# Kernel optimization log

Measured on AMD Instinct MI355X. Metric: run time of the kernel, lower is better.

Reference implementation:

```python
import jax, jax.numpy as jnp
from jax import lax
import numpy as np

# Straight-through-estimator sign (standard BNN binarization):
# fwd: sign(x) with sign(0)=+1; bwd: pass gradient where |x|<=1 (hardtanh STE).
@jax.custom_vjp
def sign_ste(x):
    return jnp.where(x >= 0, 1.0, -1.0).astype(x.dtype)

def _sign_fwd(x):
    return sign_ste(x), x

def _sign_bwd(x, g):
    return (g * (jnp.abs(x) <= 1.0).astype(g.dtype),)

sign_ste.defvjp(_sign_fwd, _sign_bwd)

EPS = 1e-5  # BatchNorm eps (torch default)

def bn4(x, g, b):  # BatchNorm2d, training-mode batch stats, x: [N,C,H,W]
    m = x.mean((0, 2, 3), keepdims=True)
    v = x.var((0, 2, 3), keepdims=True)
    return g[None, :, None, None] * (x - m) * lax.rsqrt(v + EPS) + b[None, :, None, None]

def bn1(x, g, b):  # BatchNorm1d, x: [N,C]
    m = x.mean(0, keepdims=True)
    v = x.var(0, keepdims=True)
    return g * (x - m) * lax.rsqrt(v + EPS) + b

def bconv(x, W, b, first):
    # BinarizedConv2d: binarize weights always; binarize input except first layer.
    xb = x if first else sign_ste(x)
    y = lax.conv_general_dilated(xb, sign_ste(W), (1, 1), [(1, 1), (1, 1)],
                                 dimension_numbers=('NCHW', 'OIHW', 'NCHW'))
    return y + b[None, :, None, None]

def maxpool2(x):
    return lax.reduce_window(x, -jnp.inf, lax.max, (1, 1, 2, 2), (1, 1, 2, 2), 'VALID')

def ht(x):  # Hardtanh
    return jnp.clip(x, -1.0, 1.0)

CONV_CH = [(3, 64), (64, 128), (128, 256), (256, 256), (256, 512), (512, 512), (512, 512), (512, 512)]
LIN_CH = [(512, 512), (512, 512), (512, 10)]
POOL_AFTER = (0, 1, 3, 5, 7)  # conv indices followed by MaxPool2d

def setup_inputs():
    key = jax.random.key(0)
    ks = iter(jax.random.split(key, 64))
    d = {"x": jax.random.normal(next(ks), (256, 3, 32, 32), jnp.float32)}
    for i, (ci, co) in enumerate(CONV_CH):
        d[f"cw{i}"] = jax.random.normal(next(ks), (co, ci, 3, 3), jnp.float32) * 0.1
        d[f"cb{i}"] = jnp.zeros((co,), jnp.float32)
        d[f"cg{i}"] = jnp.ones((co,), jnp.float32)
        d[f"ct{i}"] = jnp.zeros((co,), jnp.float32)
    for i, (ci, co) in enumerate(LIN_CH):
        d[f"lw{i}"] = jax.random.normal(next(ks), (co, ci), jnp.float32) * 0.1
        d[f"lb{i}"] = jnp.zeros((co,), jnp.float32)
        d[f"lg{i}"] = jnp.ones((co,), jnp.float32)
        d[f"lt{i}"] = jnp.zeros((co,), jnp.float32)
    return d

def _forward(x, cw, cb, cg, ct, lw, lb, lg, lt):
    h = x
    for i in range(8):
        h = bconv(h, cw[i], cb[i], i == 0)
        if i in POOL_AFTER:
            h = maxpool2(h)
        h = ht(bn4(h, cg[i], ct[i]))
    h = h.reshape(h.shape[0], -1)  # [N, 512] after 5 pools on 32x32
    for i in range(3):
        h = sign_ste(h) @ sign_ste(lw[i]).T + lb[i]  # BinarizedLinear
        h = bn1(h, lg[i], lt[i])
        if i < 2:
            h = ht(h)  # Dropout is identity in eval mode
    return jax.nn.log_softmax(h, axis=-1)

def reference(x,
              cw0, cb0, cg0, ct0, cw1, cb1, cg1, ct1, cw2, cb2, cg2, ct2,
              cw3, cb3, cg3, ct3, cw4, cb4, cg4, ct4, cw5, cb5, cg5, ct5,
              cw6, cb6, cg6, ct6, cw7, cb7, cg7, ct7,
              lw0, lb0, lg0, lt0, lw1, lb1, lg1, lt1, lw2, lb2, lg2, lt2):
    cw = [cw0, cw1, cw2, cw3, cw4, cw5, cw6, cw7]
    cb = [cb0, cb1, cb2, cb3, cb4, cb5, cb6, cb7]
    cg = [cg0, cg1, cg2, cg3, cg4, cg5, cg6, cg7]
    ct = [ct0, ct1, ct2, ct3, ct4, ct5, ct6, ct7]
    lw = [lw0, lw1, lw2]
    lb = [lb0, lb1, lb2]
    lg = [lg0, lg1, lg2]
    lt = [lt0, lt1, lt2]
    return _forward(x, cw, cb, cg, ct, lw, lb, lg, lt)
```

## Files before the change

### kernel.cpp

```cpp
#include <hip/hip_runtime.h>
#include <hip/hip_bf16.h>

typedef unsigned long long u64;

#define EPSV 1e-5

__device__ __forceinline__ int imax(int a, int b) { return a > b ? a : b; }
__device__ __forceinline__ int iclamp(int v, int lo, int hi) { return v < lo ? lo : (v > hi ? hi : v); }

struct PrepArgs {
    const float* src[10];
    u64* dst[10];
    int CW[10];
    int Co[10];
    int taps[10];
    int rowbase[11];
    u64* accs;
    int naccs;
};

__global__ __launch_bounds__(256) void prep_kernel(PrepArgs a) {
    __shared__ float buf[4608];
    const int blk = blockIdx.x;
    int z = blk * 18 + threadIdx.x;
    if (threadIdx.x < 18 && z < a.naccs) a.accs[z] = 0ULL;

    int l = 0;
    while (l < 9 && blk >= a.rowbase[l + 1]) ++l;
    const int row = blk - a.rowbase[l];
    const int CW = a.CW[l];
    const int taps = a.taps[l];
    const int nf = CW * 64 * taps;
    const float* srow = a.src[l] + (size_t)row * nf;
    for (int i = threadIdx.x; i < nf; i += 256) buf[i] = srow[i];
    __syncthreads();
    const int t = threadIdx.x;
    if (t < taps * CW) {
        u64 bits = 0;
        if (taps == 9) {
            int k = t % 9, w = t / 9;
            for (int j = 0; j < 64; ++j) bits |= (u64)(buf[(w * 64 + j) * 9 + k] >= 0.f) << j;
            a.dst[l][(size_t)(k * CW + w) * a.Co[l] + row] = bits;
        } else {
            for (int j = 0; j < 64; ++j) bits |= (u64)(buf[t * 64 + j] >= 0.f) << j;
            a.dst[l][(size_t)row * CW + t] = bits;
        }
    }
}

__global__ __launch_bounds__(256) void conv0_lane(const float* __restrict__ x,
                                                  const float* __restrict__ wgt,
                                                  float* __restrict__ out,
                                                  double* __restrict__ dacc) {
    const int lane = threadIdx.x & 63;
    const int wave = threadIdx.x >> 6;
    float ws[27];
#pragma unroll
    for (int j = 0; j < 27; ++j) ws[j] = (wgt[lane * 27 + j] >= 0.f) ? 1.f : -1.f;

    const int gp0 = blockIdx.x * 32;
    const int n = gp0 >> 8;
    const int ypA = (gp0 >> 4) & 15;
    const int yb = 2 * ypA - 1;

    __shared__ float simg[3][6][34];
    const float* xb = x + (size_t)n * 3072;
    for (int t = threadIdx.x; t < 612; t += 256) {
        int ci = t / 204;
        int rem = t % 204;
        int r = rem / 34;
        int cc = rem % 34;
        int yy = yb + r;
        int xx = cc - 1;
        float v = 0.f;
        if ((unsigned)yy < 32u && (unsigned)xx < 32u) v = xb[(ci * 32 + yy) * 32 + xx];
        simg[ci][r][cc] = v;
    }
    __syncthreads();

    double s1 = 0.0, s2 = 0.0;
#pragma unroll 2
    for (int pi = 0; pi < 8; ++pi) {
        const int lp = wave * 8 + pi;
        const int gp = gp0 + lp;
        const int xp = lp & 15;
        const int rbase = 2 * (lp >> 4);
        const int cbase = 2 * xp;
        float win[3][4][4];
#pragma unroll
        for (int ci = 0; ci < 3; ++ci)
#pragma unroll
            for (int r = 0; r < 4; ++r)
#pragma unroll
                for (int c = 0; c < 4; ++c) win[ci][r][c] = simg[ci][rbase + r][cbase + c];
        float a00 = 0.f, a01 = 0.f, a10 = 0.f, a11 = 0.f;
#pragma unroll
        for (int ci = 0; ci < 3; ++ci)
#pragma unroll
            for (int ky = 0; ky < 3; ++ky)
#pragma unroll
                for (int kx = 0; kx < 3; ++kx) {
                    float wv = ws[ci * 9 + ky * 3 + kx];
                    a00 += win[ci][ky][kx] * wv;
                    a01 += win[ci][ky][kx + 1] * wv;
                    a10 += win[ci][ky + 1][kx] * wv;
                    a11 += win[ci][ky + 1][kx + 1] * wv;
                }
        float val = fmaxf(fmaxf(a00, a01), fmaxf(a10, a11));
        out[(size_t)gp * 64 + lane] = val;
        s1 += (double)val;
        s2 += (double)val * (double)val;
    }
    __shared__ double sh1[4][64], sh2[4][64];
    sh1[wave][lane] = s1;
    sh2[wave][lane] = s2;
    __syncthreads();
    if (threadIdx.x < 64) {
        double t1 = 0.0, t2 = 0.0;
#pragma unroll
        for (int r = 0; r < 4; ++r) { t1 += sh1[r][threadIdx.x]; t2 += sh2[r][threadIdx.x]; }
        double* sh = dacc + (size_t)(blockIdx.x & 7) * 1024;
        atomicAdd(&sh[2 * threadIdx.x], t1);
        atomicAdd(&sh[2 * threadIdx.x + 1], t2);
    }
}

__global__ __launch_bounds__(256) void bnpack_f(const float* __restrict__ in,
                                                const double* __restrict__ dacc,
                                                const float* __restrict__ g,
                                                const float* __restrict__ b,
                                                u64* __restrict__ act, int count) {
    __shared__ float2 sthr[64];
    if (threadIdx.x < 64) {
        int i = threadIdx.x;
        double S1 = 0.0, S2 = 0.0;
#pragma unroll
        for (int s = 0; s < 8; ++s) {
            S1 += dacc[s * 1024 + 2 * i];
            S2 += dacc[s * 1024 + 2 * i + 1];
        }
        double m = S1 / count;
        double var = S2 / count - m * m;
        double sc = (double)g[i] / sqrt(var + EPSV);
        float2 r;
        if (sc == 0.0) r = make_float2(b[i] >= 0.f ? -3.0e38f : 3.0e38f, 1.f);
        else {
            double t = m - (double)b[i] / sc;
            r = make_float2((float)t, sc > 0.0 ? 1.f : -1.f);
        }
        sthr[i] = r;
    }
    __syncthreads();
    int tid = blockIdx.x * 256 + threadIdx.x;
    int part = tid & 3;
    int word = tid >> 2;
    const float4* r4 = (const float4*)(in + (size_t)word * 64 + part * 16);
    u64 bits = 0;
#pragma unroll
    for (int q = 0; q < 4; ++q) {
        float4 v = r4[q];
        float vv[4] = {v.x, v.y, v.z, v.w};
#pragma unroll
        for (int u = 0; u < 4; ++u) {
            int c = part * 16 + q * 4 + u;
            float2 t = sthr[c];
            bool bit = (t.y > 0.f) ? (vv[u] >= t.x) : (vv[u] <= t.x);
            bits |= (u64)bit << c;
        }
    }
    bits |= __shfl_xor(bits, 1);
    bits |= __shfl_xor(bits, 2);
    if (part == 0) act[word] = bits;
}

__global__ __launch_bounds__(256) void bnpack_i(const short* __restrict__ in,
                                                const u64* __restrict__ iacc,
                                                const float* __restrict__ g,
                                                const float* __restrict__ b,
                                                u64* __restrict__ act, int Co, int wshift,
                                                int count) {
    __shared__ int2 sthr[520];
    for (int i = threadIdx.x; i < Co; i += 256) {
        long long S1 = 0, S2 = 0;
#pragma unroll
        for (int s = 0; s < 8; ++s) {
            S1 += (long long)iacc[s * 1024 + 2 * i];
            S2 += (long long)iacc[s * 1024 + 2 * i + 1];
        }
        double m = (double)S1 / count;
        double var = (double)S2 / count - m * m;
        double sc = (double)g[i] / sqrt(var + EPSV);
        int2 r;
        if (sc == 0.0) r = make_int2(b[i] >= 0.f ? (int)0x80000000 : 0x7fffffff, 0);
        else {
            double t = m - (double)b[i] / sc;
            if (t > 1.0e9) t = 1.0e9;
            if (t < -1.0e9) t = -1.0e9;
            r = (sc > 0.0) ? make_int2((int)ceil(t), 0) : make_int2((int)floor(t), 1);
        }
        sthr[(i >> 6) * 65 + (i & 63)] = r;
    }
    __syncthreads();
    int tid = blockIdx.x * 256 + threadIdx.x;
    int part = tid & 3;
    int word = tid >> 2;
    int w = word & ((1 << wshift) - 1);
    int pix = word >> wshift;
    const int4* r4 = (const int4*)(in + (size_t)pix * Co + (w << 6) + part * 16);
    u64 bits = 0;
#pragma unroll
    for (int q = 0; q < 2; ++q) {
        int4 v = r4[q];
        int words4[4] = {v.x, v.y, v.z, v.w};
#pragma unroll
        for (int u = 0; u < 4; ++u) {
#pragma unroll
            for (int h = 0; h < 2; ++h) {
                int c = part * 16 + q * 8 + u * 2 + h;
                int val = (int)(short)((h == 0) ? (words4[u] & 0xffff) : ((unsigned)words4[u] >> 16));
                int2 t = sthr[w * 65 + c];
                bool bit = t.y ? (val <= t.x) : (val >= t.x);
                bits |= (u64)bit << c;
            }
        }
    }
    bits |= __shfl_xor(bits, 1);
    bits |= __shfl_xor(bits, 2);
    if (part == 0) act[word] = bits;
}

template <int CW, int HIN, bool POOL, int WC, bool INTERIOR>
__device__ __forceinline__ void row_accum(const u64* __restrict__ inb,
                                          const u64* __restrict__ wpkT, int Co, int co,
                                          const int* yoff, const bool* ry, int* acc) {
    constexpr int HP = POOL ? HIN / 2 : HIN;
    constexpr int WS = POOL ? 4 : 3;
    constexpr int NA = POOL ? 4 : 1;
#pragma unroll 1
    for (int w0 = 0; w0 < CW; w0 += WC) {
        u64 wg[9 * WC];
#pragma unroll
        for (int k = 0; k < 9; ++k)
#pragma unroll
            for (int w = 0; w < WC; ++w)
                wg[k * WC + w] = wpkT[(size_t)(k * CW + w0 + w) * Co + co];
        u64 cur[WS][WS][WC];
#pragma unroll
        for (int d = 0; d < WS; ++d) {
            int cc = d - 1;
            int ccc = cc < 0 ? 0 : cc;
#pragma unroll
            for (int r = 0; r < WS; ++r) {
                const u64* p = inb + yoff[r] + ccc * CW + w0;
                if (WC == 1) {
                    cur[r][d][0] = p[0];
                } else {
                    ulonglong2 v = *(const ulonglong2*)p;
                    cur[r][d][0] = v.x;
                    cur[r][d][1] = v.y;
                }
            }
        }
#pragma unroll
        for (int xp = 0; xp < HP; ++xp) {
            if constexpr (POOL) {
#pragma unroll
                for (int py = 0; py < 2; ++py)
#pragma unroll
                    for (int qx = 0; qx < 2; ++qx)
#pragma unroll
                        for (int ky = 0; ky < 3; ++ky)
#pragma unroll
                            for (int kx = 0; kx < 3; ++kx) {
                                int d = qx + kx;
                                int cc = 2 * xp + d - 1;
                                if (cc >= 0 && cc < HIN) {
#pragma unroll
                                    for (int w = 0; w < WC; ++w) {
                                        int pcv = 64 - 2 * (int)__popcll(cur[py + ky][d][w] ^
                                                                         wg[(ky * 3 + kx) * WC + w]);
                                        if constexpr (INTERIOR)
                                            acc[xp * NA + py * 2 + qx] += pcv;
                                        else
                                            acc[xp * NA + py * 2 + qx] += ry[py + ky] ? pcv : 0;
                                    }
                                }
                            }
            } else {
#pragma unroll
                for (int ky = 0; ky < 3; ++ky)
#pragma unroll
                    for (int kx = 0; kx < 3; ++kx) {
                        int cc = xp + kx - 1;
                        if (cc >= 0 && cc < HIN) {
#pragma unroll
                            for (int w = 0; w < WC; ++w) {
                                int pcv = 64 - 2 * (int)__popcll(cur[ky][kx][w] ^
                                                                 wg[(ky * 3 + kx) * WC + w]);
                                if constexpr (INTERIOR)
                                    acc[xp] += pcv;
                                else
                                    acc[xp] += ry[ky] ? pcv : 0;
                            }
                        }
                    }
            }
            if (xp < HP - 1) {
                if constexpr (POOL) {
#pragma unroll
                    for (int r = 0; r < WS; ++r)
#pragma unroll
                        for (int w = 0; w < WC; ++w) {
                            cur[r][0][w] = cur[r][2][w];
                            cur[r][1][w] = cur[r][3][w];
                        }
#pragma unroll
                    for (int dd = 2; dd < 4; ++dd) {
                        int cc = 2 * (xp + 1) + dd - 1;
                        int ccc = cc >= HIN ? HIN - 1 : cc;
#pragma unroll
                        for (int r = 0; r < WS; ++r) {
                            const u64* p = inb + yoff[r] + ccc * CW + w0;
                            if (WC == 1) {
                                cur[r][dd][0] = p[0];
                            } else {
                                ulonglong2 v = *(const ulonglong2*)p;
                                cur[r][dd][0] = v.x;
                                cur[r][dd][1] = v.y;
                            }
                        }
                    }
                } else {
#pragma unroll
                    for (int r = 0; r < WS; ++r)
#pragma unroll
                        for (int w = 0; w < WC; ++w) {
                            cur[r][0][w] = cur[r][1][w];
                            cur[r][1][w] = cur[r][2][w];
                        }
                    int cc = xp + 2;
                    int ccc = cc >= HIN ? HIN - 1 : cc;
#pragma unroll
                    for (int r = 0; r < WS; ++r) {
                        const u64* p = inb + yoff[r] + ccc * CW + w0;
                        if (WC == 1) {
                            cur[r][2][0] = p[0];
                        } else {
                            ulonglong2 v = *(const ulonglong2*)p;
                            cur[r][2][0] = v.x;
                            cur[r][2][1] = v.y;
                        }
                    }
                }
            }
        }
    }
}

template <int CW, int HIN, bool POOL, int WC>
__global__ __launch_bounds__(256) void bconv_row(const u64* __restrict__ in,
                                                 const u64* __restrict__ wpkT,
                                                 short* __restrict__ out,
                                                 u64* __restrict__ iacc, int Co) {
    constexpr int HP = POOL ? HIN / 2 : HIN;
    constexpr int WS = POOL ? 4 : 3;
    constexpr int NA = POOL ? 4 : 1;
    const int lane = threadIdx.x & 63;
    const int co = blockIdx.y * 64 + lane;
    const int grow = blockIdx.x * 4 + (threadIdx.x >> 6);
    const int n = grow / HP;
    const int yp = grow % HP;
    const int y0 = (POOL ? 2 * yp : yp) - 1;
    const u64* inb = in + (size_t)n * (HIN * HIN * CW);
    int yoff[WS];
    bool ry[WS];
#pragma unroll
    for (int r = 0; r < WS; ++r) {
        int y = y0 + r;
        ry[r] = (unsigned)y < (unsigned)HIN;
        int yc = iclamp(y, 0, HIN - 1);
        yoff[r] = yc * HIN * CW;
    }
    int acc[HP * NA];
#pragma unroll
    for (int i = 0; i < HP * NA; ++i) acc[i] = 0;

    if (yp > 0 && yp < HP - 1)
        row_accum<CW, HIN, POOL, WC, true>(inb, wpkT, Co, co, yoff, ry, acc);
    else
        row_accum<CW, HIN, POOL, WC, false>(inb, wpkT, Co, co, yoff, ry, acc);

    int s1 = 0;
    long long s2 = 0;
    short* orow = out + (size_t)grow * HP * Co + co;
#pragma unroll
    for (int xp = 0; xp < HP; ++xp) {
        int ival;
        if constexpr (POOL)
            ival = imax(imax(acc[xp * 4], acc[xp * 4 + 1]), imax(acc[xp * 4 + 2], acc[xp * 4 + 3]));
        else
            ival = acc[xp];
        orow[(size_t)xp * Co] = (short)ival;
        s1 += ival;
        s2 += (long long)ival * ival;
    }

    __shared__ u64 sacc[128];
    if (threadIdx.x < 128) sacc[threadIdx.x] = 0ULL;
    __syncthreads();
    atomicAdd(&sacc[lane], (u64)(long long)s1);
    atomicAdd(&sacc[64 + lane], (u64)s2);
    __syncthreads();
    u64* sh = iacc + (size_t)(blockIdx.x & 7) * 1024;
    if (threadIdx.x < 64)
        atomicAdd(&sh[2 * (blockIdx.y * 64 + threadIdx.x)], sacc[threadIdx.x]);
    else if (threadIdx.x < 128)
        atomicAdd(&sh[2 * (blockIdx.y * 64 + threadIdx.x - 64) + 1], sacc[threadIdx.x]);
}

template <int CW, int HIN, bool POOL>
__global__ __launch_bounds__(256) void bconv_tiny(const u64* __restrict__ in,
                                                  const u64* __restrict__ wpkT,
                                                  short* __restrict__ out,
                                                  u64* __restrict__ iacc, int Co) {
    constexpr int NPX = HIN * HIN;
    constexpr int HP = POOL ? HIN / 2 : HIN;
    const int lane = threadIdx.x & 63;
    const int co = blockIdx.y * 64 + lane;
    const int n = blockIdx.x * 4 + (threadIdx.x >> 6);
    const u64* inb = in + (size_t)n * CW * NPX;
    int acc[NPX];
#pragma unroll
    for (int i = 0; i < NPX; ++i) acc[i] = 0;

#pragma unroll 2
    for (int w = 0; w < CW; ++w) {
        u64 win[NPX];
#pragma unroll
        for (int i = 0; i < NPX; ++i) win[i] = inb[i * CW + w];
#pragma unroll
        for (int k = 0; k < 9; ++k) {
            u64 wb = wpkT[(size_t)(k * CW + w) * Co + co];
            const int ky = k / 3, kx = k % 3;
#pragma unroll
            for (int py = 0; py < HIN; ++py)
#pragma unroll
                for (int px = 0; px < HIN; ++px) {
                    const int yy = py + ky - 1, xx = px + kx - 1;
                    if (yy >= 0 && yy < HIN && xx >= 0 && xx < HIN)
                        acc[py * HIN + px] += 64 - 2 * (int)__popcll(win[yy * HIN + xx] ^ wb);
                }
        }
    }

    short vals[HP * HP];
    if constexpr (POOL) {
#pragma unroll
        for (int py = 0; py < HP; ++py)
#pragma unroll
            for (int px = 0; px < HP; ++px)
                vals[py * HP + px] = (short)imax(
                    imax(acc[(2 * py) * HIN + 2 * px], acc[(2 * py) * HIN + 2 * px + 1]),
                    imax(acc[(2 * py + 1) * HIN + 2 * px], acc[(2 * py + 1) * HIN + 2 * px + 1]));
    } else {
#pragma unroll
        for (int i = 0; i < NPX; ++i) vals[i] = (short)acc[i];
    }
#pragma unroll
    for (int p = 0; p < HP * HP; ++p) out[(size_t)(n * HP * HP + p) * Co + co] = vals[p];

    long long s1 = 0, s2 = 0;
#pragma unroll
    for (int p = 0; p < HP * HP; ++p) {
        s1 += vals[p];
        s2 += (long long)vals[p] * vals[p];
    }
    __shared__ u64 sacc[128];
    if (threadIdx.x < 128) sacc[threadIdx.x] = 0ULL;
    __syncthreads();
    atomicAdd(&sacc[lane], (u64)s1);
    atomicAdd(&sacc[64 + lane], (u64)s2);
    __syncthreads();
    u64* sh = iacc + (size_t)(blockIdx.x & 7) * 1024;
    if (threadIdx.x < 64)
        atomicAdd(&sh[2 * (blockIdx.y * 64 + threadIdx.x)], sacc[threadIdx.x]);
    else if (threadIdx.x < 128)
        atomicAdd(&sh[2 * (blockIdx.y * 64 + threadIdx.x - 64) + 1], sacc[threadIdx.x]);
}

__global__ __launch_bounds__(256) void lin_kernel(const u64* __restrict__ hp,
                                                  const u64* __restrict__ wp,
                                                  const float* __restrict__ lb,
                                                  const float* __restrict__ g,
                                                  const float* __restrict__ bta,
                                                  float* __restrict__ z, int O, int applyHt) {
    int o = blockIdx.x;
    int n = threadIdx.x;
    const u64* hr = hp + n * 8;
    const u64* wr = wp + o * 8;
    int s = 0;
#pragma unroll
    for (int w = 0; w < 8; ++w) s += (int)__popcll(hr[w] ^ wr[w]);
    float val = (float)(512 - 2 * s) + lb[o];
    __shared__ double sh1[256], sh2[256];
    sh1[n] = (double)val;
    sh2[n] = (double)val * (double)val;
    __syncthreads();
    for (int st = 128; st > 0; st >>= 1) {
        if (n < st) {
            sh1[n] += sh1[n + st];
            sh2[n] += sh2[n + st];
        }
        __syncthreads();
    }
    __shared__ float sm, siv;
    if (n == 0) {
        double m = sh1[0] / 256.0;
        double var = sh2[0] / 256.0 - m * m;
        sm = (float)m;
        siv = (float)(1.0 / sqrt(var + EPSV));
    }
    __syncthreads();
    float zz = g[o] * (val - sm) * siv + bta[o];
    if (applyHt) zz = fminf(1.f, fmaxf(-1.f, zz));
    z[(size_t)n * O + o] = zz;
}

__global__ void pack_rows(const float* __restrict__ z, u64* __restrict__ hp) {
    int tid = blockIdx.x * 256 + threadIdx.x;
    int part = tid & 3;
    int word = tid >> 2;
    int ww = word & 7;
    int n = word >> 3;
    const float4* r4 = (const float4*)(z + (size_t)n * 512 + (ww << 6) + part * 16);
    u64 bits = 0;
#pragma unroll
    for (int q = 0; q < 4; ++q) {
        float4 v = r4[q];
        float vv[4] = {v.x, v.y, v.z, v.w};
#pragma unroll
        for (int u = 0; u < 4; ++u) bits |= (u64)(vv[u] >= 0.f) << (part * 16 + q * 4 + u);
    }
    bits |= __shfl_xor(bits, 1);
    bits |= __shfl_xor(bits, 2);
    if (part == 0) hp[word] = bits;
}

__global__ void lsm_kernel(const float* __restrict__ z, float* __restrict__ out) {
    int n = blockIdx.x * 64 + threadIdx.x;
    if (n >= 256) return;
    float v[10];
    float m = -1e30f;
#pragma unroll
    for (int i = 0; i < 10; ++i) {
        v[i] = z[n * 10 + i];
        m = fmaxf(m, v[i]);
    }
    float s = 0.f;
#pragma unroll
    for (int i = 0; i < 10; ++i) s += expf(v[i] - m);
    float ls = logf(s);
#pragma unroll
    for (int i = 0; i < 10; ++i) out[n * 10 + i] = v[i] - m - ls;
}

extern "C" void kernel_launch(void* const* d_in, const int* in_sizes, int n_in, void* d_out,
                              int out_size, void* d_ws, size_t ws_size, hipStream_t stream) {
    (void)in_sizes; (void)n_in; (void)out_size; (void)ws_size;
    const float* x = (const float*)d_in[0];
    const float *cw[8], *cb[8], *cg[8], *ct[8];
    for (int i = 0; i < 8; ++i) {
        cw[i] = (const float*)d_in[1 + 4 * i];
        cb[i] = (const float*)d_in[2 + 4 * i];
        cg[i] = (const float*)d_in[3 + 4 * i];
        ct[i] = (const float*)d_in[4 + 4 * i];
    }
    const float *lw[3], *lb[3], *lg[3], *lt[3];
    for (int i = 0; i < 3; ++i) {
        lw[i] = (const float*)d_in[33 + 4 * i];
        lb[i] = (const float*)d_in[34 + 4 * i];
        lg[i] = (const float*)d_in[35 + 4 * i];
        lt[i] = (const float*)d_in[36 + 4 * i];
    }

    static const int CIs[8] = {3, 64, 128, 256, 256, 512, 512, 512};
    static const int COs[8] = {64, 128, 256, 256, 512, 512, 512, 512};
    static const int HPs[8] = {16, 8, 8, 4, 4, 2, 2, 1};

    char* ws = (char*)d_ws;
    size_t off = 0;
    auto alloc = [&](size_t bytes) -> void* {
        void* p = ws + off;
        off += (bytes + 255) & ~(size_t)255;
        return p;
    };

    u64* wpkT[8] = {};
    for (int i = 1; i < 8; ++i) wpkT[i] = (u64*)alloc((size_t)COs[i] * 9 * (CIs[i] / 64) * 8);
    u64* wpl[3];
    int LO[3] = {512, 512, 10};
    for (int i = 0; i < 3; ++i) wpl[i] = (u64*)alloc((size_t)LO[i] * 8 * 8);
    u64* act[8];
    for (int i = 0; i < 8; ++i) act[i] = (u64*)alloc((size_t)256 * (COs[i] / 64) * HPs[i] * HPs[i] * 8);
    u64* fcs0 = (u64*)alloc(2048 * 8);
    u64* fcs1 = (u64*)alloc(2048 * 8);
    float* out0 = (float*)alloc((size_t)65536 * 64 * 4);
    short* i16A = (short*)alloc((size_t)16384 * 256 * 2);
    short* i16B = (short*)alloc((size_t)16384 * 256 * 2);
    float* z0 = (float*)alloc((size_t)256 * 512 * 4);
    float* z1 = (float*)alloc((size_t)256 * 512 * 4);
    float* z2 = (float*)alloc((size_t)256 * 10 * 4);
    u64* accs = (u64*)alloc((size_t)8 * 8 * 1024 * 8);
    double* dacc0 = (double*)accs;
    auto iacc = [&](int layer) { return accs + (size_t)layer * 8192; };

    PrepArgs pa;
    int rb = 0;
    for (int i = 1; i < 8; ++i) {
        int e = i - 1;
        pa.src[e] = cw[i];
        pa.dst[e] = wpkT[i];
        pa.CW[e] = CIs[i] / 64;
        pa.Co[e] = COs[i];
        pa.taps[e] = 9;
        pa.rowbase[e] = rb;
        rb += COs[i];
    }
    for (int i = 0; i < 3; ++i) {
        int e = 7 + i;
        pa.src[e] = lw[i];
        pa.dst[e] = wpl[i];
        pa.CW[e] = 8;
        pa.Co[e] = LO[i];
        pa.taps[e] = 1;
        pa.rowbase[e] = rb;
        rb += LO[i];
    }
    pa.rowbase[10] = rb;
    pa.accs = accs;
    pa.naccs = 8 * 8 * 1024;
    prep_kernel<<<rb, 256, 0, stream>>>(pa);

    conv0_lane<<<2048, 256, 0, stream>>>(x, cw[0], out0, dacc0);
    bnpack_f<<<1024, 256, 0, stream>>>(out0, dacc0, cg[0], ct[0], act[0], 65536);

    bconv_row<1, 16, true, 1><<<dim3(512, 2), 256, 0, stream>>>(act[0], wpkT[1], i16A, iacc(1), 128);
    bnpack_i<<<512, 256, 0, stream>>>(i16A, iacc(1), cg[1], ct[1], act[1], 128, 1, 16384);

    bconv_row<2, 8, false, 2><<<dim3(512, 4), 256, 0, stream>>>(act[1], wpkT[2], i16B, iacc(2), 256);
    bnpack_i<<<1024, 256, 0, stream>>>(i16B, iacc(2), cg[2], ct[2], act[2], 256, 2, 16384);

    bconv_row<4, 8, true, 2><<<dim3(256, 4), 256, 0, stream>>>(act[2], wpkT[3], i16A, iacc(3), 256);
    bnpack_i<<<256, 256, 0, stream>>>(i16A, iacc(3), cg[3], ct[3], act[3], 256, 2, 4096);

    bconv_row<4, 4, false, 2><<<dim3(256, 8), 256, 0, stream>>>(act[3], wpkT[4], i16B, iacc(4), 512);
    bnpack_i<<<512, 256, 0, stream>>>(i16B, iacc(4), cg[4], ct[4], act[4], 512, 3, 4096);

    bconv_tiny<8, 4, true><<<dim3(64, 8), 256, 0, stream>>>(act[4], wpkT[5], i16A, iacc(5), 512);
    bnpack_i<<<128, 256, 0, stream>>>(i16A, iacc(5), cg[5], ct[5], act[5], 512, 3, 1024);

    bconv_tiny<8, 2, false><<<dim3(64, 8), 256, 0, stream>>>(act[5], wpkT[6], i16B, iacc(6), 512);
    bnpack_i<<<128, 256, 0, stream>>>(i16B, iacc(6), cg[6], ct[6], act[6], 512, 3, 1024);

    bconv_tiny<8, 2, true><<<dim3(64, 8), 256, 0, stream>>>(act[6], wpkT[7], i16A, iacc(7), 512);
    bnpack_i<<<32, 256, 0, stream>>>(i16A, iacc(7), cg[7], ct[7], act[7], 512, 3, 256);

    lin_kernel<<<512, 256, 0, stream>>>(act[7], wpl[0], lb[0], lg[0], lt[0], z0, 512, 1);
    pack_rows<<<32, 256, 0, stream>>>(z0, fcs0);
    lin_kernel<<<512, 256, 0, stream>>>(fcs0, wpl[1], lb[1], lg[1], lt[1], z1, 512, 1);
    pack_rows<<<32, 256, 0, stream>>>(z1, fcs1);
    lin_kernel<<<10, 256, 0, stream>>>(fcs1, wpl[2], lb[2], lg[2], lt[2], z2, 10, 0);
    lsm_kernel<<<4, 64, 0, stream>>>(z2, (float*)d_out);
}
```

Before: 393.8 us.

## Restructure conv0 sliding window, count-only popcount accumulation, fuse linear tail kernels

conv0 now stages weights in shared memory and lets each wave slide a register window along a row, reusing overlapping columns instead of reloading the full window per pixel. The binary conv kernels accumulate raw popcounts and apply the 64*CW*taps - 2*cnt correction once per output, which drops the per-tap arithmetic. The linear layers write sign bits straight into packed words with atomicOr, so the pack_rows kernels go away, and the last linear layer is merged with BN and log_softmax into a single block. The accumulator-zeroing in prep is widened to also clear the packed FC buffers.

After: 425.8 us. +8.1%, slower.

```diff
diff --git a/kernel.cpp b/kernel.cpp
--- a/kernel.cpp
+++ b/kernel.cpp
@@ -22,8 +22,8 @@
 __global__ __launch_bounds__(256) void prep_kernel(PrepArgs a) {
     __shared__ float buf[4608];
     const int blk = blockIdx.x;
-    int z = blk * 18 + threadIdx.x;
-    if (threadIdx.x < 18 && z < a.naccs) a.accs[z] = 0ULL;
+    int z = blk * 19 + threadIdx.x;
+    if (threadIdx.x < 19 && z < a.naccs) a.accs[z] = 0ULL;
 
     int l = 0;
     while (l < 9 && blk >= a.rowbase[l + 1]) ++l;
@@ -54,16 +54,17 @@
                                                   double* __restrict__ dacc) {
     const int lane = threadIdx.x & 63;
     const int wave = threadIdx.x >> 6;
-    float ws[27];
-#pragma unroll
-    for (int j = 0; j < 27; ++j) ws[j] = (wgt[lane * 27 + j] >= 0.f) ? 1.f : -1.f;
+
+    __shared__ __align__(16) float simg[3 * 6 * 34];
+    __shared__ float swgt[64 * 27];
 
     const int gp0 = blockIdx.x * 32;
     const int n = gp0 >> 8;
     const int ypA = (gp0 >> 4) & 15;
     const int yb = 2 * ypA - 1;
 
-    __shared__ float simg[3][6][34];
+    for (int t = threadIdx.x; t < 1728; t += 256) swgt[t] = wgt[t];
+
     const float* xb = x + (size_t)n * 3072;
     for (int t = threadIdx.x; t < 612; t += 256) {
         int ci = t / 204;
@@ -74,25 +75,35 @@
         int xx = cc - 1;
         float v = 0.f;
         if ((unsigned)yy < 32u && (unsigned)xx < 32u) v = xb[(ci * 32 + yy) * 32 + xx];
-        simg[ci][r][cc] = v;
-    }
-    __syncthreads();
+        simg[(ci * 6 + r) * 34 + cc] = v;
+    }
+    __syncthreads();
+
+    float ws[27];
+#pragma unroll
+    for (int j = 0; j < 27; ++j) ws[j] = (swgt[lane * 27 + j] >= 0.f) ? 1.f : -1.f;
+
+    const int wr = wave >> 1;
+    const int xh = (wave & 1) * 8;
+    const int rb = 2 * wr;
+
+    float win[3][4][4];
+#pragma unroll
+    for (int ci = 0; ci < 3; ++ci)
+#pragma unroll
+        for (int r = 0; r < 4; ++r) {
+            const float2* p = (const float2*)&simg[(ci * 6 + rb + r) * 34 + 2 * xh];
+            float2 a = p[0], b = p[1];
+            win[ci][r][0] = a.x;
+            win[ci][r][1] = a.y;
+            win[ci][r][2] = b.x;
+            win[ci][r][3] = b.y;
+        }
 
     double s1 = 0.0, s2 = 0.0;
-#pragma unroll 2
-    for (int pi = 0; pi < 8; ++pi) {
-        const int lp = wave * 8 + pi;
-        const int gp = gp0 + lp;
-        const int xp = lp & 15;
-        const int rbase = 2 * (lp >> 4);
-        const int cbase = 2 * xp;
-        float win[3][4][4];
-#pragma unroll
-        for (int ci = 0; ci < 3; ++ci)
-#pragma unroll
-            for (int r = 0; r < 4; ++r)
-#pragma unroll
-                for (int c = 0; c < 4; ++c) win[ci][r][c] = simg[ci][rbase + r][cbase + c];
+#pragma unroll
+    for (int i = 0; i < 8; ++i) {
+        const int xp = xh + i;
         float a00 = 0.f, a01 = 0.f, a10 = 0.f, a11 = 0.f;
 #pragma unroll
         for (int ci = 0; ci < 3; ++ci)
@@ -107,10 +118,24 @@
                     a11 += win[ci][ky + 1][kx + 1] * wv;
                 }
         float val = fmaxf(fmaxf(a00, a01), fmaxf(a10, a11));
+        const int gp = gp0 + wr * 16 + xp;
         out[(size_t)gp * 64 + lane] = val;
         s1 += (double)val;
         s2 += (double)val * (double)val;
-    }
+        if (i < 7) {
+#pragma unroll
+            for (int ci = 0; ci < 3; ++ci)
+#pragma unroll
+                for (int r = 0; r < 4; ++r) {
+                    win[ci][r][0] = win[ci][r][2];
+                    win[ci][r][1] = win[ci][r][3];
+                    float2 nb = *(const float2*)&simg[(ci * 6 + rb + r) * 34 + 2 * xp + 4];
+                    win[ci][r][2] = nb.x;
+                    win[ci][r][3] = nb.y;
+                }
+        }
+    }
+
     __shared__ double sh1[4][64], sh2[4][64];
     sh1[wave][lane] = s1;
     sh2[wave][lane] = s2;
@@ -232,7 +257,7 @@
 template <int CW, int HIN, bool POOL, int WC, bool INTERIOR>
 __device__ __forceinline__ void row_accum(const u64* __restrict__ inb,
                                           const u64* __restrict__ wpkT, int Co, int co,
-                                          const int* yoff, const bool* ry, int* acc) {
+                                          const int* yoff, const bool* ry, int* cnt) {
     constexpr int HP = POOL ? HIN / 2 : HIN;
     constexpr int WS = POOL ? 4 : 3;
     constexpr int NA = POOL ? 4 : 1;
@@ -277,12 +302,10 @@
                                 if (cc >= 0 && cc < HIN) {
 #pragma unroll
                                     for (int w = 0; w < WC; ++w) {
-                                        int pcv = 64 - 2 * (int)__popcll(cur[py + ky][d][w] ^
-                                                                         wg[(ky * 3 + kx) * WC + w]);
-                                        if constexpr (INTERIOR)
-                                            acc[xp * NA + py * 2 + qx] += pcv;
-                                        else
-                                            acc[xp * NA + py * 2 + qx] += ry[py + ky] ? pcv : 0;
+                                        if (INTERIOR || ry[py + ky])
+                                            cnt[xp * NA + py * 2 + qx] +=
+                                                (int)__popcll(cur[py + ky][d][w] ^
+                                                              wg[(ky * 3 + kx) * WC + w]);
                                     }
                                 }
                             }
@@ -295,12 +318,9 @@
                         if (cc >= 0 && cc < HIN) {
 #pragma unroll
                             for (int w = 0; w < WC; ++w) {
-                                int pcv = 64 - 2 * (int)__popcll(cur[ky][kx][w] ^
-                                                                 wg[(ky * 3 + kx) * WC + w]);
-                                if constexpr (INTERIOR)
-                                    acc[xp] += pcv;
-                                else
-                                    acc[xp] += ry[ky] ? pcv : 0;
+                                if (INTERIOR || ry[ky])
+                                    cnt[xp] += (int)__popcll(cur[ky][kx][w] ^
+                                                             wg[(ky * 3 + kx) * WC + w]);
                             }
                         }
                     }
@@ -381,14 +401,17 @@
         int yc = iclamp(y, 0, HIN - 1);
         yoff[r] = yc * HIN * CW;
     }
-    int acc[HP * NA];
-#pragma unroll
-    for (int i = 0; i < HP * NA; ++i) acc[i] = 0;
+    int cnt[HP * NA];
+#pragma unroll
+    for (int i = 0; i < HP * NA; ++i) cnt[i] = 0;
 
     if (yp > 0 && yp < HP - 1)
-        row_accum<CW, HIN, POOL, WC, true>(inb, wpkT, Co, co, yoff, ry, acc);
+        row_accum<CW, HIN, POOL, WC, true>(inb, wpkT, Co, co, yoff, ry, cnt);
     else
-        row_accum<CW, HIN, POOL, WC, false>(inb, wpkT, Co, co, yoff, ry, acc);
+        row_accum<CW, HIN, POOL, WC, false>(inb, wpkT, Co, co, yoff, ry, cnt);
+
+    const int nr0 = (int)ry[0] + (int)ry[1] + (int)ry[2];
+    const int nr1 = POOL ? ((int)ry[1] + (int)ry[2] + (int)ry[WS - 1]) : 0;
 
     int s1 = 0;
     long long s2 = 0;
@@ -396,10 +419,25 @@
 #pragma unroll
     for (int xp = 0; xp < HP; ++xp) {
         int ival;
-        if constexpr (POOL)
-            ival = imax(imax(acc[xp * 4], acc[xp * 4 + 1]), imax(acc[xp * 4 + 2], acc[xp * 4 + 3]));
-        else
-            ival = acc[xp];
+        if constexpr (POOL) {
+            int best = -2147483647;
+#pragma unroll
+            for (int py = 0; py < 2; ++py) {
+                const int nrv = py ? nr1 : nr0;
+#pragma unroll
+                for (int qx = 0; qx < 2; ++qx) {
+                    int ncols = 3;
+                    if (xp == 0 && qx == 0) ncols = 2;
+                    if (xp == HP - 1 && qx == 1) ncols = 2;
+                    int v = 64 * CW * nrv * ncols - 2 * cnt[xp * NA + py * 2 + qx];
+                    best = imax(best, v);
+                }
+            }
+            ival = best;
+        } else {
+            const int ncols = (xp == 0 || xp == HIN - 1) ? 2 : 3;
+            ival = 64 * CW * nr0 * ncols - 2 * cnt[xp];
+        }
         orow[(size_t)xp * Co] = (short)ival;
         s1 += ival;
         s2 += (long long)ival * ival;
@@ -429,9 +467,9 @@
     const int co = blockIdx.y * 64 + lane;
     const int n = blockIdx.x * 4 + (threadIdx.x >> 6);
     const u64* inb = in + (size_t)n * CW * NPX;
-    int acc[NPX];
-#pragma unroll
-    for (int i = 0; i < NPX; ++i) acc[i] = 0;
+    int cnt[NPX];
+#pragma unroll
+    for (int i = 0; i < NPX; ++i) cnt[i] = 0;
 
 #pragma unroll 2
     for (int w = 0; w < CW; ++w) {
@@ -448,10 +486,20 @@
                 for (int px = 0; px < HIN; ++px) {
                     const int yy = py + ky - 1, xx = px + kx - 1;
                     if (yy >= 0 && yy < HIN && xx >= 0 && xx < HIN)
-                        acc[py * HIN + px] += 64 - 2 * (int)__popcll(win[yy * HIN + xx] ^ wb);
+                        cnt[py * HIN + px] += (int)__popcll(win[yy * HIN + xx] ^ wb);
                 }
         }
     }
+
+    int fin[NPX];
+#pragma unroll
+    for (int py = 0; py < HIN; ++py)
+#pragma unroll
+        for (int px = 0; px < HIN; ++px) {
+            const int nk = ((py == 0 || py == HIN - 1) ? 2 : 3) *
+                           ((px == 0 || px == HIN - 1) ? 2 : 3);
+            fin[py * HIN + px] = 64 * CW * nk - 2 * cnt[py * HIN + px];
+        }
 
     short vals[HP * HP];
     if constexpr (POOL) {
@@ -460,11 +508,11 @@
 #pragma unroll
             for (int px = 0; px < HP; ++px)
                 vals[py * HP + px] = (short)imax(
-                    imax(acc[(2 * py) * HIN + 2 * px], acc[(2 * py) * HIN + 2 * px + 1]),
-                    imax(acc[(2 * py + 1) * HIN + 2 * px], acc[(2 * py + 1) * HIN + 2 * px + 1]));
+                    imax(fin[(2 * py) * HIN + 2 * px], fin[(2 * py) * HIN + 2 * px + 1]),
+                    imax(fin[(2 * py + 1) * HIN + 2 * px], fin[(2 * py + 1) * HIN + 2 * px + 1]));
     } else {
 #pragma unroll
-        for (int i = 0; i < NPX; ++i) vals[i] = (short)acc[i];
+        for (int i = 0; i < NPX; ++i) vals[i] = (short)fin[i];
     }
 #pragma unroll
     for (int p = 0; p < HP * HP; ++p) out[(size_t)(n * HP * HP + p) * Co + co] = vals[p];
@@ -493,7 +541,7 @@
                                                   const float* __restrict__ lb,
                                                   const float* __restrict__ g,
                                                   const float* __restrict__ bta,
-                                                  float* __restrict__ z, int O, int applyHt) {
+                                                  u64* __restrict__ op) {
     int o = blockIdx.x;
     int n = threadIdx.x;
     const u64* hr = hp + n * 8;
@@ -522,46 +570,65 @@
     }
     __syncthreads();
     float zz = g[o] * (val - sm) * siv + bta[o];
-    if (applyHt) zz = fminf(1.f, fmaxf(-1.f, zz));
-    z[(size_t)n * O + o] = zz;
-}
-
-__global__ void pack_rows(const float* __restrict__ z, u64* __restrict__ hp) {
-    int tid = blockIdx.x * 256 + threadIdx.x;
-    int part = tid & 3;
-    int word = tid >> 2;
-    int ww = word & 7;
-    int n = word >> 3;
-    const float4* r4 = (const float4*)(z + (size_t)n * 512 + (ww << 6) + part * 16);
-    u64 bits = 0;
-#pragma unroll
-    for (int q = 0; q < 4; ++q) {
-        float4 v = r4[q];
-        float vv[4] = {v.x, v.y, v.z, v.w};
-#pragma unroll
-        for (int u = 0; u < 4; ++u) bits |= (u64)(vv[u] >= 0.f) << (part * 16 + q * 4 + u);
-    }
-    bits |= __shfl_xor(bits, 1);
-    bits |= __shfl_xor(bits, 2);
-    if (part == 0) hp[word] = bits;
-}
-
-__global__ void lsm_kernel(const float* __restrict__ z, float* __restrict__ out) {
-    int n = blockIdx.x * 64 + threadIdx.x;
-    if (n >= 256) return;
+    if (zz >= 0.f) atomicOr(&op[(size_t)n * 8 + (o >> 6)], 1ULL << (o & 63));
+}
+
+__global__ __launch_bounds__(256) void lin2_lsm(const u64* __restrict__ hp,
+                                                const u64* __restrict__ wp,
+                                                const float* __restrict__ lb,
+                                                const float* __restrict__ g,
+                                                const float* __restrict__ bta,
+                                                float* __restrict__ out) {
+    const int n = threadIdx.x;
+    const int lane = n & 63;
+    const int wave = n >> 6;
+    u64 h[8];
+#pragma unroll
+    for (int w = 0; w < 8; ++w) h[w] = hp[n * 8 + w];
     float v[10];
-    float m = -1e30f;
-#pragma unroll
-    for (int i = 0; i < 10; ++i) {
-        v[i] = z[n * 10 + i];
-        m = fmaxf(m, v[i]);
-    }
-    float s = 0.f;
-#pragma unroll
-    for (int i = 0; i < 10; ++i) s += expf(v[i] - m);
-    float ls = logf(s);
-#pragma unroll
-    for (int i = 0; i < 10; ++i) out[n * 10 + i] = v[i] - m - ls;
+#pragma unroll
+    for (int o = 0; o < 10; ++o) {
+        int s = 0;
+#pragma unroll
+        for (int w = 0; w < 8; ++w) s += (int)__popcll(h[w] ^ wp[o * 8 + w]);
+        v[o] = (float)(512 - 2 * s) + lb[o];
+    }
+    __shared__ double w1[4][10], w2[4][10];
+#pragma unroll
+    for (int o = 0; o < 10; ++o) {
+        double a = (double)v[o];
+        double b = a * a;
+#pragma unroll
+        for (int off = 32; off > 0; off >>= 1) {
+            a += __shfl_xor(a, off);
+            b += __shfl_xor(b, off);
+        }
+        if (lane == 0) {
+            w1[wave][o] = a;
+            w2[wave][o] = b;
+        }
+    }
+    __syncthreads();
+    float z[10];
+#pragma unroll
+    for (int o = 0; o < 10; ++o) {
+        double S1 = w1[0][o] + w1[1][o] + w1[2][o] + w1[3][o];
+        double S2 = w2[0][o] + w2[1][o] + w2[2][o] + w2[3][o];
+        double m = S1 / 256.0;
+        double var = S2 / 256.0 - m * m;
+        float sm = (float)m;
+        float siv = (float)(1.0 / sqrt(var + EPSV));
+        z[o] = g[o] * (v[o] - sm) * siv + bta[o];
+    }
+    float mx = z[0];
+#pragma unroll
+    for (int o = 1; o < 10; ++o) mx = fmaxf(mx, z[o]);
+    float se = 0.f;
+#pragma unroll
+    for (int o = 0; o < 10; ++o) se += expf(z[o] - mx);
+    float ls = logf(se);
+#pragma unroll
+    for (int o = 0; o < 10; ++o) out[n * 10 + o] = z[o] - mx - ls;
 }
 
 extern "C" void kernel_launch(void* const* d_in, const int* in_sizes, int n_in, void* d_out,
@@ -595,6 +662,12 @@
         return p;
     };
 
+    u64* accs = (u64*)alloc((size_t)8 * 8 * 1024 * 8);
+    u64* fcs0 = (u64*)alloc(2048 * 8);
+    u64* fcs1 = (u64*)alloc(2048 * 8);
+    double* dacc0 = (double*)accs;
+    auto iacc = [&](int layer) { return accs + (size_t)layer * 8192; };
+
     u64* wpkT[8] = {};
     for (int i = 1; i < 8; ++i) wpkT[i] = (u64*)alloc((size_t)COs[i] * 9 * (CIs[i] / 64) * 8);
     u64* wpl[3];
@@ -602,17 +675,9 @@
     for (int i = 0; i < 3; ++i) wpl[i] = (u64*)alloc((size_t)LO[i] * 8 * 8);
     u64* act[8];
     for (int i = 0; i < 8; ++i) act[i] = (u64*)alloc((size_t)256 * (COs[i] / 64) * HPs[i] * HPs[i] * 8);
-    u64* fcs0 = (u64*)alloc(2048 * 8);
-    u64* fcs1 = (u64*)alloc(2048 * 8);
     float* out0 = (float*)alloc((size_t)65536 * 64 * 4);
     short* i16A = (short*)alloc((size_t)16384 * 256 * 2);
     short* i16B = (short*)alloc((size_t)16384 * 256 * 2);
-    float* z0 = (float*)alloc((size_t)256 * 512 * 4);
-    float* z1 = (float*)alloc((size_t)256 * 512 * 4);
-    float* z2 = (float*)alloc((size_t)256 * 10 * 4);
-    u64* accs = (u64*)alloc((size_t)8 * 8 * 1024 * 8);
-    double* dacc0 = (double*)accs;
-    auto iacc = [&](int layer) { return accs + (size_t)layer * 8192; };
 
     PrepArgs pa;
     int rb = 0;
@@ -638,7 +703,7 @@
     }
     pa.rowbase[10] = rb;
     pa.accs = accs;
-    pa.naccs = 8 * 8 * 1024;
+    pa.naccs = 8 * 8 * 1024 + 2048 + 2048;
     prep_kernel<<<rb, 256, 0, stream>>>(pa);
 
     conv0_lane<<<2048, 256, 0, stream>>>(x, cw[0], out0, dacc0);
@@ -665,10 +730,7 @@
     bconv_tiny<8, 2, true><<<dim3(64, 8), 256, 0, stream>>>(act[6], wpkT[7], i16A, iacc(7), 512);
     bnpack_i<<<32, 256, 0, stream>>>(i16A, iacc(7), cg[7], ct[7], act[7], 512, 3, 256);
 
-    lin_kernel<<<512, 256, 0, stream>>>(act[7], wpl[0], lb[0], lg[0], lt[0], z0, 512, 1);
-    pack_rows<<<32, 256, 0, stream>>>(z0, fcs0);
-    lin_kernel<<<512, 256, 0, stream>>>(fcs0, wpl[1], lb[1], lg[1], lt[1], z1, 512, 1);
-    pack_rows<<<32, 256, 0, stream>>>(z1, fcs1);
-    lin_kernel<<<10, 256, 0, stream>>>(fcs1, wpl[2], lb[2], lg[2], lt[2], z2, 10, 0);
-    lsm_kernel<<<4, 64, 0, stream>>>(z2, (float*)d_out);
-}
+    lin_kernel<<<512, 256, 0, stream>>>(act[7], wpl[0], lb[0], lg[0], lt[0], fcs0);
+    lin_kernel<<<512, 256, 0, stream>>>(fcs0, wpl[1], lb[1], lg[1], lt[1], fcs1);
+    lin2_lsm<<<1, 256, 0, stream>>>(fcs1, wpl[2], lb[2], lg[2], lt[2], (float*)d_out);
+}
```
